# Optimization experiments

Measured on AMD Instinct MI355X. Metric: run time of the kernel, lower is better.

Reference implementation:

```python
import jax, jax.numpy as jnp
import numpy as np

B = 16384          # batch (parallel envs)
D_OBS = 512        # num_actor_obs
A = 32             # num_actions
E = 8              # num_experts
K = 2              # top_k
GH = [256, 128]    # gating hidden dims
EH = [1024, 512, 256]  # expert hidden dims


def _linear_init(key, fan_in, fan_out, extra=()):
    kw, kb = jax.random.split(key)
    scale = 1.0 / np.sqrt(fan_in)
    w = jax.random.uniform(kw, extra + (fan_in, fan_out), jnp.float32, -scale, scale)
    b = jax.random.uniform(kb, extra + (fan_out,), jnp.float32, -scale, scale)
    return w, b


def setup_inputs() -> dict:
    key = jax.random.key(0)
    ks = jax.random.split(key, 8)
    obs = jax.random.normal(ks[0], (B, D_OBS), jnp.float32)
    # gating network: D_OBS -> 256 -> 128 -> E
    gw1, gb1 = _linear_init(ks[1], D_OBS, GH[0])
    gw2, gb2 = _linear_init(ks[2], GH[0], GH[1])
    gw3, gb3 = _linear_init(ks[3], GH[1], E)
    # experts (stacked over expert axis): D_OBS -> 1024 -> 512 -> 256 -> A
    ew1, eb1 = _linear_init(ks[4], D_OBS, EH[0], (E,))
    ew2, eb2 = _linear_init(ks[5], EH[0], EH[1], (E,))
    ew3, eb3 = _linear_init(ks[6], EH[1], EH[2], (E,))
    ew4, eb4 = _linear_init(ks[7], EH[2], A, (E,))
    return {
        "observations": obs,
        "gw1": gw1, "gb1": gb1, "gw2": gw2, "gb2": gb2, "gw3": gw3, "gb3": gb3,
        "ew1": ew1, "eb1": eb1, "ew2": ew2, "eb2": eb2,
        "ew3": ew3, "eb3": eb3, "ew4": ew4, "eb4": eb4,
    }


def reference(observations, gw1, gb1, gw2, gb2, gw3, gb3,
              ew1, eb1, ew2, eb2, ew3, eb3, ew4, eb4):
    elu = jax.nn.elu
    # --- gating network ---
    g = elu(observations @ gw1 + gb1)
    g = elu(g @ gw2 + gb2)
    gate_logits = g @ gw3 + gb3                      # [B, E]
    gate_probs = jax.nn.softmax(gate_logits, axis=-1)
    # --- top-k selection and renormalization ---
    topk_w, topk_idx = jax.lax.top_k(gate_probs, K)  # [B, K]
    topk_w = topk_w / jnp.sum(topk_w, axis=-1, keepdims=True)
    # --- run all experts as batched GEMMs (same math as masked dispatch) ---
    h = elu(jnp.einsum('bi,eio->beo', observations, ew1) + eb1)  # [B, E, 1024]
    h = elu(jnp.einsum('beo,eoh->beh', h, ew2) + eb2)            # [B, E, 512]
    h = elu(jnp.einsum('beh,ehf->bef', h, ew3) + eb3)            # [B, E, 256]
    expert_out = jnp.einsum('bef,efa->bea', h, ew4) + eb4        # [B, E, A]
    # --- weighted combine over selected experts ---
    onehot = jax.nn.one_hot(topk_idx, E, dtype=topk_w.dtype)     # [B, K, E]
    combine_w = jnp.einsum('bk,bke->be', topk_w, onehot)         # [B, E]
    action_mean = jnp.einsum('be,bea->ba', combine_w, expert_out)  # [B, A]
    return action_mean
```

## Files before the change

kernel.cpp:

```cpp
#include <hip/hip_runtime.h>
#include <hip/hip_bf16.h>

typedef __bf16 v8bf __attribute__((ext_vector_type(8)));
typedef float  v4f  __attribute__((ext_vector_type(4)));

#define B_ROWS 16384
#define NSLOTS 32768
#define MAXTILES 264

#define OFF_W1T   0u
#define OFF_W2T   8388608u
#define OFF_W3T   16777216u
#define OFF_W4T   18874368u
#define OFF_META  19005440u
#define OFF_SEL   19009536u
#define OFF_W01   19075072u
#define OFF_ROWL  19206144u
#define OFF_WL    19337216u
#define OFF_Q     19468288u
#define OFF_G1    OFF_Q
#define OFF_G2    (OFF_Q + 16777216u)
#define OFF_X1    OFF_Q
#define OFF_H2    OFF_Q
#define OFF_EO    OFF_Q
#define OFF_H1    (OFF_Q + 33554432u)
#define OFF_H3    OFF_H1
#define WS_NEED   (OFF_H1 + 67108864u)


__device__ __forceinline__ void gload_lds16(const void* g, void* l) {
  __builtin_amdgcn_global_load_lds(
      (const __attribute__((address_space(1))) void*)g,
      (__attribute__((address_space(3))) void*)l, 16, 0, 0);
}

__device__ __forceinline__ float elu_f(float x) {
  return x > 0.f ? x : expm1f(x);
}

__global__ __launch_bounds__(256) void transpose_convert(
    const float* __restrict__ in, __hip_bfloat16* __restrict__ outp, int R, int C) {
  __shared__ __align__(16) float tile[32][33];
  int e = blockIdx.z;
  const float* src = in + (size_t)e * R * C;
  __hip_bfloat16* dst = outp + (size_t)e * R * C;
  int r0 = blockIdx.x * 32, c0 = blockIdx.y * 32;
  int tr = threadIdx.x >> 5, tc = threadIdx.x & 31;
#pragma unroll
  for (int q = 0; q < 4; ++q)
    tile[tr + 8*q][tc] = src[(size_t)(r0 + tr + 8*q) * C + c0 + tc];
  __syncthreads();
#pragma unroll
  for (int q = 0; q < 4; ++q)
    dst[(size_t)(c0 + tr + 8*q) * R + r0 + tc] = __float2bfloat16(tile[tc][tr + 8*q]);
}

__global__ __launch_bounds__(256) void sgemm_elu(
    const float* __restrict__ A, const float* __restrict__ Bm,
    const float* __restrict__ bias, float* __restrict__ C,
    int M, int N, int K) {
  __shared__ __align__(16) float sA[16][132];
  __shared__ __align__(16) float sB[16][68];
  int tid = threadIdx.x;
  int tx = tid & 15, ty = tid >> 4;
  int m0 = blockIdx.x * 128, n0 = blockIdx.y * 64;
  float acc[8][4] = {};
  for (int k0 = 0; k0 < K; k0 += 16) {
    {
      int m = tid >> 1, ks = (tid & 1) * 8;
      const float* ap = &A[(size_t)(m0 + m) * K + k0 + ks];
      float4 v0 = *(const float4*)ap;
      float4 v1 = *(const float4*)(ap + 4);
      sA[ks+0][m] = v0.x; sA[ks+1][m] = v0.y; sA[ks+2][m] = v0.z; sA[ks+3][m] = v0.w;
      sA[ks+4][m] = v1.x; sA[ks+5][m] = v1.y; sA[ks+6][m] = v1.z; sA[ks+7][m] = v1.w;
    }
    {
      int kr = tid >> 4, nn = (tid & 15) * 4;
      *(float4*)&sB[kr][nn] = *(const float4*)&Bm[(size_t)(k0 + kr) * N + n0 + nn];
    }
    __syncthreads();
#pragma unroll
    for (int kk = 0; kk < 16; ++kk) {
      float a[8], b[4];
      *(float4*)&a[0] = *(const float4*)&sA[kk][ty*8];
      *(float4*)&a[4] = *(const float4*)&sA[kk][ty*8+4];
      *(float4*)&b[0] = *(const float4*)&sB[kk][tx*4];
#pragma unroll
      for (int i = 0; i < 8; ++i)
#pragma unroll
        for (int j = 0; j < 4; ++j)
          acc[i][j] = fmaf(a[i], b[j], acc[i][j]);
    }
    __syncthreads();
  }
  float bs[4];
#pragma unroll
  for (int j = 0; j < 4; ++j) bs[j] = bias[n0 + tx*4 + j];
#pragma unroll
  for (int i = 0; i < 8; ++i) {
    int m = m0 + ty*8 + i;
    float4 o;
    o.x = elu_f(acc[i][0] + bs[0]);
    o.y = elu_f(acc[i][1] + bs[1]);
    o.z = elu_f(acc[i][2] + bs[2]);
    o.w = elu_f(acc[i][3] + bs[3]);
    *(float4*)&C[(size_t)m * N + n0 + tx*4] = o;
  }
}

__global__ __launch_bounds__(256) void gate3_topk(
    const float* __restrict__ G2, const float* __restrict__ gw3,
    const float* __restrict__ gb3, int* __restrict__ sel01,
    float2* __restrict__ w01, int* __restrict__ meta) {
  __shared__ __align__(16) float g2t[64][132];
  __shared__ __align__(16) float w3[1024];
  __shared__ float b3[8];
  __shared__ int lc[8];
  int tid = threadIdx.x;
  int row0 = blockIdx.x * 64;
  {
    int r = tid >> 5, f = (tid & 31) * 4;
#pragma unroll
    for (int rr = 0; rr < 64; rr += 8)
      *(float4*)&g2t[r + rr][f] = *(const float4*)&G2[(size_t)(row0 + r + rr) * 128 + f];
  }
  ((float4*)w3)[tid] = ((const float4*)gw3)[tid];
  if (tid < 8) { b3[tid] = gb3[tid]; lc[tid] = 0; }
  __syncthreads();
  if (tid < 64) {
    int row = row0 + tid;
    float lg[8];
#pragma unroll
    for (int e = 0; e < 8; ++e) lg[e] = b3[e];
    for (int k = 0; k < 128; ++k) {
      float x = g2t[tid][k];
#pragma unroll
      for (int e = 0; e < 8; ++e) lg[e] = fmaf(x, w3[k*8 + e], lg[e]);
    }
    float mx = lg[0];
#pragma unroll
    for (int e = 1; e < 8; ++e) mx = fmaxf(mx, lg[e]);
    float p[8], s = 0.f;
#pragma unroll
    for (int e = 0; e < 8; ++e) { p[e] = expf(lg[e] - mx); s += p[e]; }
    float inv = 1.f / s;
#pragma unroll
    for (int e = 0; e < 8; ++e) p[e] *= inv;
    int i0 = 0; float v0 = p[0];
#pragma unroll
    for (int e = 1; e < 8; ++e) if (p[e] > v0) { v0 = p[e]; i0 = e; }
    int i1 = -1; float v1 = -1.f;
#pragma unroll
    for (int e = 0; e < 8; ++e) if (e != i0 && p[e] > v1) { v1 = p[e]; i1 = e; }
    float sw = 1.f / (v0 + v1);
    sel01[row] = i0 | (i1 << 8);
    w01[row] = make_float2(v0 * sw, v1 * sw);
    atomicAdd(&lc[i0], 1);
    atomicAdd(&lc[i1], 1);
  }
  __syncthreads();
  if (tid < 8) atomicAdd(&meta[1 + tid], lc[tid]);
}

__global__ void build_tiles(int* __restrict__ meta) {
  if (threadIdx.x != 0) return;
  int base = 0, nt = 0;
  for (int e = 0; e < 8; ++e) {
    int c = meta[1 + e];
    meta[17 + e] = base;
    for (int j = 0; j < c; j += 128) {
      meta[32 + nt]  = e;
      meta[296 + nt] = base + j;
      meta[560 + nt] = (c - j < 128) ? (c - j) : 128;
      nt++;
    }
    base += c;
  }
  meta[0] = nt;
}

__global__ __launch_bounds__(256) void scatter_rows(
    const int* __restrict__ sel01, float2* __restrict__ w01,
    int* __restrict__ meta, int* __restrict__ rowlist, float* __restrict__ wlist) {
  __shared__ int lc[8];
  __shared__ int gb[8];
  int tid = threadIdx.x;
  if (tid < 8) lc[tid] = 0;
  __syncthreads();
  int row = blockIdx.x * 256 + tid;
  int s = sel01[row];
  int e0 = s & 255, e1 = (s >> 8) & 255;
  float2 w = w01[row];
  int l0 = atomicAdd(&lc[e0], 1);
  int l1 = atomicAdd(&lc[e1], 1);
  __syncthreads();
  if (tid < 8) gb[tid] = atomicAdd(&meta[9 + tid], lc[tid]);
  __syncthreads();
  int s0 = meta[17 + e0] + gb[e0] + l0;
  int s1 = meta[17 + e1] + gb[e1] + l1;
  rowlist[s0] = row; wlist[s0] = w.x;
  rowlist[s1] = row; wlist[s1] = w.y;
  ((int2*)w01)[row] = make_int2(s0, s1);
}

__global__ __launch_bounds__(256) void gather_convert(
    const float* __restrict__ obs, const int* __restrict__ rowlist,
    __hip_bfloat16* __restrict__ X1) {
  int tid = threadIdx.x;
  int slot = blockIdx.x * 4 + (tid >> 6);
  int l = tid & 63;
  int row = rowlist[slot];
  const float* src = obs + (size_t)row * 512 + l * 8;
  float4 a = *(const float4*)src;
  float4 b = *(const float4*)(src + 4);
  union { __hip_bfloat16 h[8]; uint4 u; } t;
  t.h[0] = __float2bfloat16(a.x); t.h[1] = __float2bfloat16(a.y);
  t.h[2] = __float2bfloat16(a.z); t.h[3] = __float2bfloat16(a.w);
  t.h[4] = __float2bfloat16(b.x); t.h[5] = __float2bfloat16(b.y);
  t.h[6] = __float2bfloat16(b.z); t.h[7] = __float2bfloat16(b.w);
  *(uint4*)(X1 + (size_t)slot * 512 + l * 8) = t.u;
}

__global__ __launch_bounds__(256) void moe_gemm(
    const __hip_bfloat16* __restrict__ A, const __hip_bfloat16* __restrict__ BT,
    const float* __restrict__ bias, __hip_bfloat16* __restrict__ C,
    const int* __restrict__ meta, int N, int K) {
  int t = blockIdx.x;
  if (t >= meta[0]) return;
  int e    = meta[32 + t];
  int m0   = meta[296 + t];
  int rows = meta[560 + t];
  int n0   = blockIdx.y * 128;

  __shared__ __align__(16) __hip_bfloat16 sA[128 * 32];
  __shared__ __align__(16) __hip_bfloat16 sB[128 * 32];

  int tid = threadIdx.x;
  int w = tid >> 6, l = tid & 63;
  int lr = l >> 2;
  int lk = (l & 3) * 8;
  int wm = w >> 1, wn = w & 1;
  int ml = l & 15, kq = l >> 4;

  const __hip_bfloat16* BTe = BT + (size_t)e * N * K;
  v4f acc[4][4] = {};

  for (int k0 = 0; k0 < K; k0 += 32) {
#pragma unroll
    for (int it = 0; it < 2; ++it) {
      int r = it * 64 + w * 16 + lr;
      int gr = m0 + (r < rows ? r : rows - 1);
      gload_lds16(A + (size_t)gr * K + k0 + lk, &sA[(it * 64 + w * 16) * 32]);
    }
#pragma unroll
    for (int it = 0; it < 2; ++it) {
      int r = it * 64 + w * 16 + lr;
      gload_lds16(BTe + (size_t)(n0 + r) * K + k0 + lk, &sB[(it * 64 + w * 16) * 32]);
    }
    __syncthreads();
    v8bf af[4], bf[4];
#pragma unroll
    for (int i = 0; i < 4; ++i)
      af[i] = *(const v8bf*)&sA[(wm * 64 + i * 16 + ml) * 32 + kq * 8];
#pragma unroll
    for (int j = 0; j < 4; ++j)
      bf[j] = *(const v8bf*)&sB[(wn * 64 + j * 16 + ml) * 32 + kq * 8];
#pragma unroll
    for (int i = 0; i < 4; ++i)
#pragma unroll
      for (int j = 0; j < 4; ++j)
        acc[i][j] = __builtin_amdgcn_mfma_f32_16x16x32_bf16(af[i], bf[j], acc[i][j], 0, 0, 0);
    __syncthreads();
  }

  int rl0 = kq * 4;
#pragma unroll
  for (int j = 0; j < 4; ++j) {
    int col = n0 + wn * 64 + j * 16 + ml;
    float bs = bias[(size_t)e * N + col];
#pragma unroll
    for (int i = 0; i < 4; ++i) {
#pragma unroll
      for (int r = 0; r < 4; ++r) {
        int rl = wm * 64 + i * 16 + rl0 + r;
        if (rl < rows) {
          float v = elu_f(acc[i][j][r] + bs);
          C[(size_t)(m0 + rl) * N + col] = __float2bfloat16(v);
        }
      }
    }
  }
}

__global__ __launch_bounds__(256) void l4_gemm(
    const __hip_bfloat16* __restrict__ H3, const __hip_bfloat16* __restrict__ W4T,
    const float* __restrict__ eb4, const int* __restrict__ meta,
    float* __restrict__ EO) {
  int t = blockIdx.x;
  if (t >= meta[0]) return;
  int e = meta[32 + t], m0 = meta[296 + t], rows = meta[560 + t];
  __shared__ __align__(16) __hip_bfloat16 sW[32 * 264];
  int tid = threadIdx.x;
  {
    const uint4* src = (const uint4*)(W4T + (size_t)e * 8192);
#pragma unroll
    for (int q = 0; q < 4; ++q) {
      int c = tid + 256 * q;
      int r = c >> 5, col = (c & 31) * 8;
      *(uint4*)&sW[r * 264 + col] = src[c];
    }
  }
  __syncthreads();
  int w = tid >> 6, l = tid & 63;
  int ml = l & 15, kq = l >> 4;
  v4f acc[2][2] = {};
  const __hip_bfloat16* Abase = H3 + (size_t)m0 * 256;
#pragma unroll
  for (int k0 = 0; k0 < 256; k0 += 32) {
    v8bf af[2], bf[2];
#pragma unroll
    for (int i = 0; i < 2; ++i) {
      int r = w * 32 + i * 16 + ml;
      int rr = r < rows ? r : 0;
      af[i] = *(const v8bf*)(Abase + (size_t)rr * 256 + k0 + kq * 8);
    }
#pragma unroll
    for (int j = 0; j < 2; ++j)
      bf[j] = *(const v8bf*)&sW[(j * 16 + ml) * 264 + k0 + kq * 8];
#pragma unroll
    for (int i = 0; i < 2; ++i)
#pragma unroll
      for (int j = 0; j < 2; ++j)
        acc[i][j] = __builtin_amdgcn_mfma_f32_16x16x32_bf16(af[i], bf[j], acc[i][j], 0, 0, 0);
  }
#pragma unroll
  for (int j = 0; j < 2; ++j) {
    int col = j * 16 + ml;
    float bs = eb4[e * 32 + col];
#pragma unroll
    for (int i = 0; i < 2; ++i) {
#pragma unroll
      for (int r = 0; r < 4; ++r) {
        int rl = w * 32 + i * 16 + kq * 4 + r;
        if (rl < rows)
          EO[(size_t)(m0 + rl) * 32 + col] = acc[i][j][r] + bs;
      }
    }
  }
}

__global__ __launch_bounds__(256) void combine_out(
    const float* __restrict__ EO, const int2* __restrict__ invmap,
    const float* __restrict__ wlist, float* __restrict__ out) {
  int gid = blockIdx.x * 256 + threadIdx.x;
  int row = gid >> 3, q = (gid & 7) * 4;
  int2 s = invmap[row];
  float w0 = wlist[s.x], w1 = wlist[s.y];
  float4 a = *(const float4*)(EO + (size_t)s.x * 32 + q);
  float4 b = *(const float4*)(EO + (size_t)s.y * 32 + q);
  float4 o;
  o.x = w0 * a.x + w1 * b.x;
  o.y = w0 * a.y + w1 * b.y;
  o.z = w0 * a.z + w1 * b.z;
  o.w = w0 * a.w + w1 * b.w;
  *(float4*)(out + (size_t)row * 32 + q) = o;
}

extern "C" void kernel_launch(void* const* d_in, const int* in_sizes, int n_in,
                              void* d_out, int out_size, void* d_ws, size_t ws_size,
                              hipStream_t stream) {
  const float* obs = (const float*)d_in[0];
  const float* gw1 = (const float*)d_in[1];
  const float* gb1 = (const float*)d_in[2];
  const float* gw2 = (const float*)d_in[3];
  const float* gb2 = (const float*)d_in[4];
  const float* gw3 = (const float*)d_in[5];
  const float* gb3 = (const float*)d_in[6];
  const float* ew1 = (const float*)d_in[7];
  const float* eb1 = (const float*)d_in[8];
  const float* ew2 = (const float*)d_in[9];
  const float* eb2 = (const float*)d_in[10];
  const float* ew3 = (const float*)d_in[11];
  const float* eb3 = (const float*)d_in[12];
  const float* ew4 = (const float*)d_in[13];
  const float* eb4 = (const float*)d_in[14];

  if (ws_size < (size_t)WS_NEED) return;

  char* ws = (char*)d_ws;
  __hip_bfloat16* W1T = (__hip_bfloat16*)(ws + OFF_W1T);
  __hip_bfloat16* W2T = (__hip_bfloat16*)(ws + OFF_W2T);
  __hip_bfloat16* W3T = (__hip_bfloat16*)(ws + OFF_W3T);
  __hip_bfloat16* W4T = (__hip_bfloat16*)(ws + OFF_W4T);
  int*    meta    = (int*)(ws + OFF_META);
  int*    sel01   = (int*)(ws + OFF_SEL);
  float2* w01     = (float2*)(ws + OFF_W01);
  int*    rowlist = (int*)(ws + OFF_ROWL);
  float*  wlist   = (float*)(ws + OFF_WL);
  float*  G1      = (float*)(ws + OFF_G1);
  float*  G2      = (float*)(ws + OFF_G2);
  __hip_bfloat16* X1 = (__hip_bfloat16*)(ws + OFF_X1);
  __hip_bfloat16* H1 = (__hip_bfloat16*)(ws + OFF_H1);
  __hip_bfloat16* H2 = (__hip_bfloat16*)(ws + OFF_H2);
  __hip_bfloat16* H3 = (__hip_bfloat16*)(ws + OFF_H3);
  float* EO       = (float*)(ws + OFF_EO);
  float* outp = (float*)d_out;

  (void)hipMemsetAsync(meta, 0, 128, stream);

  transpose_convert<<<dim3(16, 32, 8), 256, 0, stream>>>(ew1, W1T, 512, 1024);
  transpose_convert<<<dim3(32, 16, 8), 256, 0, stream>>>(ew2, W2T, 1024, 512);
  transpose_convert<<<dim3(16,  8, 8), 256, 0, stream>>>(ew3, W3T, 512, 256);
  transpose_convert<<<dim3( 8,  1, 8), 256, 0, stream>>>(ew4, W4T, 256, 32);

  sgemm_elu<<<dim3(128, 4), 256, 0, stream>>>(obs, gw1, gb1, G1, B_ROWS, 256, 512);
  sgemm_elu<<<dim3(128, 2), 256, 0, stream>>>(G1, gw2, gb2, G2, B_ROWS, 128, 256);
  gate3_topk<<<256, 256, 0, stream>>>(G2, gw3, gb3, sel01, w01, meta);
  build_tiles<<<1, 64, 0, stream>>>(meta);
  scatter_rows<<<64, 256, 0, stream>>>(sel01, w01, meta, rowlist, wlist);
  gather_convert<<<8192, 256, 0, stream>>>(obs, rowlist, X1);

  moe_gemm<<<dim3(MAXTILES, 8), 256, 0, stream>>>(X1, W1T, eb1, H1, meta, 1024, 512);
  moe_gemm<<<dim3(MAXTILES, 4), 256, 0, stream>>>(H1, W2T, eb2, H2, meta, 512, 1024);
  moe_gemm<<<dim3(MAXTILES, 2), 256, 0, stream>>>(H2, W3T, eb3, H3, meta, 256, 512);
  l4_gemm<<<MAXTILES, 256, 0, stream>>>(H3, W4T, eb4, meta, EO);
  combine_out<<<512, 256, 0, stream>>>(EO, (const int2*)w01, wlist, outp);
}
```

Measured before the change: 490.4 us.

## Fuse row gather into first expert GEMM, stage epilogue via LDS, merge transposes

The separate gather_convert kernel is removed: the first expert GEMM now reads observation rows through the rowlist, converts them to bf16 and writes them straight into shared memory, so the X1 buffer no longer makes a round trip through memory. The GEMM epilogues stage ELU outputs in LDS and write coalesced 16-byte nontemporal stores instead of scattered 2-byte stores. The grid is swapped so the N tiles of one M tile run next to each other, which may improve reuse of A rows in cache. The four weight-transpose launches become one kernel. In exchange, the A loads in the first GEMM are synchronous register loads instead of async LDS loads, which may expose more latency.

```diff
diff --git a/kernel.cpp b/kernel.cpp
--- a/kernel.cpp
+++ b/kernel.cpp
@@ -3,10 +3,12 @@
 
 typedef __bf16 v8bf __attribute__((ext_vector_type(8)));
 typedef float  v4f  __attribute__((ext_vector_type(4)));
+typedef unsigned int v4u __attribute__((ext_vector_type(4)));
 
 #define B_ROWS 16384
 #define NSLOTS 32768
 #define MAXTILES 264
+#define CSTRIDE 136
 
 #define OFF_W1T   0u
 #define OFF_W2T   8388608u
@@ -20,7 +22,6 @@
 #define OFF_Q     19468288u
 #define OFF_G1    OFF_Q
 #define OFF_G2    (OFF_Q + 16777216u)
-#define OFF_X1    OFF_Q
 #define OFF_H2    OFF_Q
 #define OFF_EO    OFF_Q
 #define OFF_H1    (OFF_Q + 33554432u)
@@ -38,13 +39,22 @@
   return x > 0.f ? x : expm1f(x);
 }
 
-__global__ __launch_bounds__(256) void transpose_convert(
-    const float* __restrict__ in, __hip_bfloat16* __restrict__ outp, int R, int C) {
+__global__ __launch_bounds__(256) void transpose_all(
+    const float* __restrict__ ew1, const float* __restrict__ ew2,
+    const float* __restrict__ ew3, const float* __restrict__ ew4,
+    __hip_bfloat16* __restrict__ W1T, __hip_bfloat16* __restrict__ W2T,
+    __hip_bfloat16* __restrict__ W3T, __hip_bfloat16* __restrict__ W4T) {
   __shared__ __align__(16) float tile[32][33];
-  int e = blockIdx.z;
-  const float* src = in + (size_t)e * R * C;
-  __hip_bfloat16* dst = outp + (size_t)e * R * C;
-  int r0 = blockIdx.x * 32, c0 = blockIdx.y * 32;
+  int b = blockIdx.x;
+  const float* src; __hip_bfloat16* dst; int R, C, gxs, tps, idx;
+  if (b < 4096)      { src = ew1; dst = W1T; R = 512;  C = 1024; gxs = 4; tps = 9; idx = b; }
+  else if (b < 8192) { src = ew2; dst = W2T; R = 1024; C = 512;  gxs = 5; tps = 9; idx = b - 4096; }
+  else if (b < 9216) { src = ew3; dst = W3T; R = 512;  C = 256;  gxs = 4; tps = 7; idx = b - 8192; }
+  else               { src = ew4; dst = W4T; R = 256;  C = 32;   gxs = 3; tps = 3; idx = b - 9216; }
+  int e = idx >> tps, tt = idx & ((1 << tps) - 1);
+  int r0 = (tt & ((1 << gxs) - 1)) * 32, c0 = (tt >> gxs) * 32;
+  src += (size_t)e * R * C;
+  dst += (size_t)e * R * C;
   int tr = threadIdx.x >> 5, tc = threadIdx.x & 31;
 #pragma unroll
   for (int q = 0; q < 4; ++q)
@@ -203,37 +213,21 @@
   ((int2*)w01)[row] = make_int2(s0, s1);
 }
 
-__global__ __launch_bounds__(256) void gather_convert(
-    const float* __restrict__ obs, const int* __restrict__ rowlist,
-    __hip_bfloat16* __restrict__ X1) {
-  int tid = threadIdx.x;
-  int slot = blockIdx.x * 4 + (tid >> 6);
-  int l = tid & 63;
-  int row = rowlist[slot];
-  const float* src = obs + (size_t)row * 512 + l * 8;
-  float4 a = *(const float4*)src;
-  float4 b = *(const float4*)(src + 4);
-  union { __hip_bfloat16 h[8]; uint4 u; } t;
-  t.h[0] = __float2bfloat16(a.x); t.h[1] = __float2bfloat16(a.y);
-  t.h[2] = __float2bfloat16(a.z); t.h[3] = __float2bfloat16(a.w);
-  t.h[4] = __float2bfloat16(b.x); t.h[5] = __float2bfloat16(b.y);
-  t.h[6] = __float2bfloat16(b.z); t.h[7] = __float2bfloat16(b.w);
-  *(uint4*)(X1 + (size_t)slot * 512 + l * 8) = t.u;
-}
-
 __global__ __launch_bounds__(256) void moe_gemm(
     const __hip_bfloat16* __restrict__ A, const __hip_bfloat16* __restrict__ BT,
     const float* __restrict__ bias, __hip_bfloat16* __restrict__ C,
     const int* __restrict__ meta, int N, int K) {
-  int t = blockIdx.x;
+  int t = blockIdx.y;
   if (t >= meta[0]) return;
   int e    = meta[32 + t];
   int m0   = meta[296 + t];
   int rows = meta[560 + t];
-  int n0   = blockIdx.y * 128;
-
-  __shared__ __align__(16) __hip_bfloat16 sA[128 * 32];
-  __shared__ __align__(16) __hip_bfloat16 sB[128 * 32];
+  int n0   = blockIdx.x * 128;
+
+  __shared__ __align__(16) char smem[CSTRIDE * 128 * 2 > 16384 ? CSTRIDE * 128 * 2 : 16384];
+  __hip_bfloat16* sA  = (__hip_bfloat16*)smem;
+  __hip_bfloat16* sB  = (__hip_bfloat16*)(smem + 8192);
+  __hip_bfloat16* cst = (__hip_bfloat16*)smem;
 
   int tid = threadIdx.x;
   int w = tid >> 6, l = tid & 63;
@@ -273,22 +267,137 @@
     __syncthreads();
   }
 
-  int rl0 = kq * 4;
-#pragma unroll
-  for (int j = 0; j < 4; ++j) {
-    int col = n0 + wn * 64 + j * 16 + ml;
-    float bs = bias[(size_t)e * N + col];
-#pragma unroll
-    for (int i = 0; i < 4; ++i) {
-#pragma unroll
-      for (int r = 0; r < 4; ++r) {
-        int rl = wm * 64 + i * 16 + rl0 + r;
-        if (rl < rows) {
-          float v = elu_f(acc[i][j][r] + bs);
-          C[(size_t)(m0 + rl) * N + col] = __float2bfloat16(v);
-        }
+  float bs[4];
+#pragma unroll
+  for (int j = 0; j < 4; ++j)
+    bs[j] = bias[(size_t)e * N + n0 + wn * 64 + j * 16 + ml];
+
+#pragma unroll
+  for (int h = 0; h < 2; ++h) {
+    if (wm == h) {
+#pragma unroll
+      for (int i = 0; i < 4; ++i)
+#pragma unroll
+        for (int j = 0; j < 4; ++j)
+#pragma unroll
+          for (int r = 0; r < 4; ++r)
+            cst[(i * 16 + kq * 4 + r) * CSTRIDE + wn * 64 + j * 16 + ml] =
+                __float2bfloat16(elu_f(acc[i][j][r] + bs[j]));
+    }
+    __syncthreads();
+#pragma unroll
+    for (int q = 0; q < 4; ++q) {
+      int z = q * 256 + tid;
+      int row = z >> 4, ch = z & 15;
+      int rl = h * 64 + row;
+      if (rl < rows) {
+        v4u v = *(const v4u*)&cst[row * CSTRIDE + ch * 8];
+        __builtin_nontemporal_store(
+            v, (v4u*)&C[(size_t)(m0 + rl) * N + n0 + ch * 8]);
       }
     }
+    __syncthreads();
+  }
+}
+
+__global__ __launch_bounds__(256) void moe_gemm_l1(
+    const float* __restrict__ obs, const __hip_bfloat16* __restrict__ BT,
+    const float* __restrict__ bias, __hip_bfloat16* __restrict__ C,
+    const int* __restrict__ rowlist, const int* __restrict__ meta, int N, int K) {
+  int t = blockIdx.y;
+  if (t >= meta[0]) return;
+  int e    = meta[32 + t];
+  int m0   = meta[296 + t];
+  int rows = meta[560 + t];
+  int n0   = blockIdx.x * 128;
+
+  __shared__ __align__(16) char smem[CSTRIDE * 128 * 2 > 16384 ? CSTRIDE * 128 * 2 : 16384];
+  __hip_bfloat16* sA  = (__hip_bfloat16*)smem;
+  __hip_bfloat16* sB  = (__hip_bfloat16*)(smem + 8192);
+  __hip_bfloat16* cst = (__hip_bfloat16*)smem;
+
+  int tid = threadIdx.x;
+  int w = tid >> 6, l = tid & 63;
+  int lr = l >> 2;
+  int lk = (l & 3) * 8;
+  int wm = w >> 1, wn = w & 1;
+  int ml = l & 15, kq = l >> 4;
+
+  int arow = (tid >> 1) < rows ? (tid >> 1) : rows - 1;
+  const float* aptr =
+      obs + (size_t)(rowlist[m0 + arow] & (B_ROWS - 1)) * 512 + (tid & 1) * 16;
+  v4u* sAdst = (v4u*)&sA[(tid >> 1) * 32 + (tid & 1) * 16];
+
+  const __hip_bfloat16* BTe = BT + (size_t)e * N * K;
+  v4f acc[4][4] = {};
+
+  for (int k0 = 0; k0 < K; k0 += 32) {
+    float4 g0 = *(const float4*)(aptr + k0);
+    float4 g1 = *(const float4*)(aptr + k0 + 4);
+    float4 g2 = *(const float4*)(aptr + k0 + 8);
+    float4 g3 = *(const float4*)(aptr + k0 + 12);
+    union { __hip_bfloat16 h[16]; v4u u[2]; } pk;
+    pk.h[0]  = __float2bfloat16(g0.x); pk.h[1]  = __float2bfloat16(g0.y);
+    pk.h[2]  = __float2bfloat16(g0.z); pk.h[3]  = __float2bfloat16(g0.w);
+    pk.h[4]  = __float2bfloat16(g1.x); pk.h[5]  = __float2bfloat16(g1.y);
+    pk.h[6]  = __float2bfloat16(g1.z); pk.h[7]  = __float2bfloat16(g1.w);
+    pk.h[8]  = __float2bfloat16(g2.x); pk.h[9]  = __float2bfloat16(g2.y);
+    pk.h[10] = __float2bfloat16(g2.z); pk.h[11] = __float2bfloat16(g2.w);
+    pk.h[12] = __float2bfloat16(g3.x); pk.h[13] = __float2bfloat16(g3.y);
+    pk.h[14] = __float2bfloat16(g3.z); pk.h[15] = __float2bfloat16(g3.w);
+    sAdst[0] = pk.u[0];
+    sAdst[1] = pk.u[1];
+#pragma unroll
+    for (int it = 0; it < 2; ++it) {
+      int r = it * 64 + w * 16 + lr;
+      gload_lds16(BTe + (size_t)(n0 + r) * K + k0 + lk, &sB[(it * 64 + w * 16) * 32]);
+    }
+    __syncthreads();
+    v8bf af[4], bf[4];
+#pragma unroll
+    for (int i = 0; i < 4; ++i)
+      af[i] = *(const v8bf*)&sA[(wm * 64 + i * 16 + ml) * 32 + kq * 8];
+#pragma unroll
+    for (int j = 0; j < 4; ++j)
+      bf[j] = *(const v8bf*)&sB[(wn * 64 + j * 16 + ml) * 32 + kq * 8];
+#pragma unroll
+    for (int i = 0; i < 4; ++i)
+#pragma unroll
+      for (int j = 0; j < 4; ++j)
+        acc[i][j] = __builtin_amdgcn_mfma_f32_16x16x32_bf16(af[i], bf[j], acc[i][j], 0, 0, 0);
+    __syncthreads();
+  }
+
+  float bs[4];
+#pragma unroll
+  for (int j = 0; j < 4; ++j)
+    bs[j] = bias[(size_t)e * N + n0 + wn * 64 + j * 16 + ml];
+
+#pragma unroll
+  for (int h = 0; h < 2; ++h) {
+    if (wm == h) {
+#pragma unroll
+      for (int i = 0; i < 4; ++i)
+#pragma unroll
+        for (int j = 0; j < 4; ++j)
+#pragma unroll
+          for (int r = 0; r < 4; ++r)
+            cst[(i * 16 + kq * 4 + r) * CSTRIDE + wn * 64 + j * 16 + ml] =
+                __float2bfloat16(elu_f(acc[i][j][r] + bs[j]));
+    }
+    __syncthreads();
+#pragma unroll
+    for (int q = 0; q < 4; ++q) {
+      int z = q * 256 + tid;
+      int row = z >> 4, ch = z & 15;
+      int rl = h * 64 + row;
+      if (rl < rows) {
+        v4u v = *(const v4u*)&cst[row * CSTRIDE + ch * 8];
+        __builtin_nontemporal_store(
+            v, (v4u*)&C[(size_t)(m0 + rl) * N + n0 + ch * 8]);
+      }
+    }
+    __syncthreads();
   }
 }
 
@@ -399,7 +508,6 @@
   float*  wlist   = (float*)(ws + OFF_WL);
   float*  G1      = (float*)(ws + OFF_G1);
   float*  G2      = (float*)(ws + OFF_G2);
-  __hip_bfloat16* X1 = (__hip_bfloat16*)(ws + OFF_X1);
   __hip_bfloat16* H1 = (__hip_bfloat16*)(ws + OFF_H1);
   __hip_bfloat16* H2 = (__hip_bfloat16*)(ws + OFF_H2);
   __hip_bfloat16* H3 = (__hip_bfloat16*)(ws + OFF_H3);
@@ -408,21 +516,17 @@
 
   (void)hipMemsetAsync(meta, 0, 128, stream);
 
-  transpose_convert<<<dim3(16, 32, 8), 256, 0, stream>>>(ew1, W1T, 512, 1024);
-  transpose_convert<<<dim3(32, 16, 8), 256, 0, stream>>>(ew2, W2T, 1024, 512);
-  transpose_convert<<<dim3(16,  8, 8), 256, 0, stream>>>(ew3, W3T, 512, 256);
-  transpose_convert<<<dim3( 8,  1, 8), 256, 0, stream>>>(ew4, W4T, 256, 32);
+  transpose_all<<<9280, 256, 0, stream>>>(ew1, ew2, ew3, ew4, W1T, W2T, W3T, W4T);
 
   sgemm_elu<<<dim3(128, 4), 256, 0, stream>>>(obs, gw1, gb1, G1, B_ROWS, 256, 512);
   sgemm_elu<<<dim3(128, 2), 256, 0, stream>>>(G1, gw2, gb2, G2, B_ROWS, 128, 256);
   gate3_topk<<<256, 256, 0, stream>>>(G2, gw3, gb3, sel01, w01, meta);
   build_tiles<<<1, 64, 0, stream>>>(meta);
   scatter_rows<<<64, 256, 0, stream>>>(sel01, w01, meta, rowlist, wlist);
-  gather_convert<<<8192, 256, 0, stream>>>(obs, rowlist, X1);
-
-  moe_gemm<<<dim3(MAXTILES, 8), 256, 0, stream>>>(X1, W1T, eb1, H1, meta, 1024, 512);
-  moe_gemm<<<dim3(MAXTILES, 4), 256, 0, stream>>>(H1, W2T, eb2, H2, meta, 512, 1024);
-  moe_gemm<<<dim3(MAXTILES, 2), 256, 0, stream>>>(H2, W3T, eb3, H3, meta, 256, 512);
+
+  moe_gemm_l1<<<dim3(8, MAXTILES), 256, 0, stream>>>(obs, W1T, eb1, H1, rowlist, meta, 1024, 512);
+  moe_gemm<<<dim3(4, MAXTILES), 256, 0, stream>>>(H1, W2T, eb2, H2, meta, 512, 1024);
+  moe_gemm<<<dim3(2, MAXTILES), 256, 0, stream>>>(H2, W3T, eb3, H3, meta, 256, 512);
   l4_gemm<<<MAXTILES, 256, 0, stream>>>(H3, W4T, eb4, meta, EO);
   combine_out<<<512, 256, 0, stream>>>(EO, (const int2*)w01, wlist, outp);
 }
```

Result: slower. 502.7 us (+2.5%).
